# Kernel optimization log

Hardware: AMD Instinct MI355X
Metric: run time of the kernel (lower is better)

The kernel has to match this reference:

```python
import jax, jax.numpy as jnp
import numpy as np

B, T, F, H1, H2 = 16384, 10, 500, 256, 100  # batch, seq_len, noise_dim/seq_len, LSTM units, GRU units


def setup_inputs() -> dict:
    key = jax.random.key(0)
    ks = jax.random.split(key, 10)
    s = 0.02  # small init so relu activations stay bounded over time steps
    return {
        "noise": jax.random.normal(ks[0], (B, T * F), dtype=jnp.float32),
        "Wx_lstm": jax.random.normal(ks[1], (F, 4 * H1), dtype=jnp.float32) * s,
        "Wh_lstm": jax.random.normal(ks[2], (H1, 4 * H1), dtype=jnp.float32) * s,
        "b_lstm": jnp.zeros((4 * H1,), dtype=jnp.float32),
        "Wx_gru": jax.random.normal(ks[3], (H1, 3 * H2), dtype=jnp.float32) * s,
        "Wh_gru": jax.random.normal(ks[4], (H2, 3 * H2), dtype=jnp.float32) * s,
        "b_in_gru": jnp.zeros((3 * H2,), dtype=jnp.float32),
        "b_rec_gru": jnp.zeros((3 * H2,), dtype=jnp.float32),
        "Wd": jax.random.normal(ks[5], (H2, T), dtype=jnp.float32) * s,
        "bd": jnp.zeros((T,), dtype=jnp.float32),
    }


def _lstm(x, Wx, Wh, b):
    # x: [T, B, F]; Keras LSTM with activation='relu', recurrent_activation='sigmoid'
    Bn = x.shape[1]
    H = Wh.shape[0]
    def step(carry, x_t):
        h, c = carry
        z = x_t @ Wx + h @ Wh + b  # [B, 4H]
        i, f, g, o = jnp.split(z, 4, axis=-1)  # Keras gate order: i, f, c, o
        i = jax.nn.sigmoid(i)
        f = jax.nn.sigmoid(f)
        g = jax.nn.relu(g)
        o = jax.nn.sigmoid(o)
        c = f * c + i * g
        h = o * jax.nn.relu(c)
        return (h, c), h
    h0 = jnp.zeros((Bn, H), dtype=x.dtype)
    (_, _), hs = jax.lax.scan(step, (h0, h0), x)
    return hs  # [T, B, H]


def _gru(x, Wx, Wh, b_in, b_rec):
    # x: [T, B, H1]; Keras GRU (reset_after=True) with activation='relu'
    Bn = x.shape[1]
    H = Wh.shape[0]
    def step(h, x_t):
        mx = x_t @ Wx + b_in    # [B, 3H]
        mh = h @ Wh + b_rec     # [B, 3H]
        xz, xr, xh = jnp.split(mx, 3, axis=-1)  # Keras gate order: z, r, h
        hz, hr, hh = jnp.split(mh, 3, axis=-1)
        z = jax.nn.sigmoid(xz + hz)
        r = jax.nn.sigmoid(xr + hr)
        hcand = jax.nn.relu(xh + r * hh)
        h = z * h + (1.0 - z) * hcand
        return h, None
    h0 = jnp.zeros((Bn, H), dtype=x.dtype)
    h_final, _ = jax.lax.scan(step, h0, x)
    return h_final  # [B, H]


def reference(noise, Wx_lstm, Wh_lstm, b_lstm, Wx_gru, Wh_gru, b_in_gru, b_rec_gru, Wd, bd):
    Fdim = Wx_lstm.shape[0]
    Tdim = noise.shape[1] // Fdim
    x = noise.reshape(noise.shape[0], Tdim, Fdim)      # Reshape((T, F))
    x = jnp.transpose(x, (1, 0, 2))                    # [T, B, F] for scan
    hs = _lstm(x, Wx_lstm, Wh_lstm, b_lstm)            # [T, B, 256]
    h = _gru(hs, Wx_gru, Wh_gru, b_in_gru, b_rec_gru)  # [B, 100]
    return jax.nn.relu(h @ Wd + bd)                    # [B, T]
```

## Files before the change

### kernel.cpp

```cpp
#include <hip/hip_runtime.h>

#define Bsz 16384
#define TT 10
#define FF 500
#define H1c 256
#define H2c 100

typedef _Float16 half8 __attribute__((ext_vector_type(8)));
typedef float floatx4 __attribute__((ext_vector_type(4)));

__device__ __forceinline__ float sigm(float x) { return 1.0f / (1.0f + __expf(-x)); }

#define GLOAD16(g, l) __builtin_amdgcn_global_load_lds( \
    (const __attribute__((address_space(1))) void*)(g), \
    (__attribute__((address_space(3))) void*)(l), 16, 0, 0)

__global__ __launch_bounds__(256)
void conv_all(const float* __restrict__ noise, _Float16* __restrict__ xc)
{
    const int idx = blockIdx.x * 256 + threadIdx.x;
    const int rb = idx >> 6;
    const int kc = (idx & 63) << 3;
    const int b = rb / 10;
    const int t = rb - b * 10;
    const float* src = noise + (size_t)rb * FF + kc;
    half8 v;
    if (kc + 8 <= FF) {
        float4 u0 = *(const float4*)src;
        float4 u1 = *(const float4*)(src + 4);
        v[0] = (_Float16)u0.x; v[1] = (_Float16)u0.y; v[2] = (_Float16)u0.z; v[3] = (_Float16)u0.w;
        v[4] = (_Float16)u1.x; v[5] = (_Float16)u1.y; v[6] = (_Float16)u1.z; v[7] = (_Float16)u1.w;
    } else {
        #pragma unroll
        for (int j = 0; j < 8; ++j)
            v[j] = (kc + j < FF) ? (_Float16)src[j] : (_Float16)0.f;
    }
    *(half8*)(xc + ((size_t)t * Bsz + b) * 512 + kc) = v;
}

__global__ __launch_bounds__(256)
void prep_lstm_w(const float* __restrict__ Wx, const float* __restrict__ Wh,
                 _Float16* __restrict__ WT)
{
    const int idx = blockIdx.x * 256 + threadIdx.x;
    const int np = idx / 768, k = idx % 768;
    const int A2 = np >> 8, B2 = (np >> 6) & 3, g = (np >> 4) & 3, u = np & 15;
    const int U = A2 * 64 + B2 * 16 + u;
    const int col = g * 256 + U;
    float v = 0.f;
    if (k < 512) { if (k < FF) v = Wx[(size_t)k * 1024 + col]; }
    else v = Wh[(size_t)(k - 512) * 1024 + col];
    WT[idx] = (_Float16)v;
}

__global__ __launch_bounds__(256)
void prep_gru_w(const float* __restrict__ Wxg, const float* __restrict__ Whg,
                _Float16* __restrict__ WT)
{
    const int idx = blockIdx.x * 256 + threadIdx.x;
    if (idx >= 384 * 384) return;
    const int np = idx / 384, k = idx % 384;
    const int nb = np / 96, rem = np % 96;
    const int wxx = rem / 48, g = (rem % 48) / 16, u = rem & 15;
    const int U = nb * 32 + wxx * 16 + u;
    float v = 0.f;
    if (U < H2c) {
        if (k < 256) v = Wxg[(size_t)k * 300 + g * H2c + U];
        else if (k - 256 < H2c) v = Whg[(size_t)(k - 256) * 300 + g * H2c + U];
    }
    WT[idx] = (_Float16)v;
}

__device__ __forceinline__
void lstm_tile(int bid, const _Float16* __restrict__ xct, const _Float16* __restrict__ WT,
               const float* __restrict__ bias,
               const _Float16* __restrict__ h_prev, const float* __restrict__ c_prev,
               _Float16* __restrict__ h_out, float* __restrict__ c_out,
               int first, _Float16* smem)
{
    _Float16* As = smem;
    _Float16* Bs = smem + 32768;

    const int tid = threadIdx.x;
    const int lane = tid & 63;
    const int w = tid >> 6;
    const int wy = w >> 2, wx = w & 3;
    const int xcd = bid & 7;
    const int nb = xcd >> 1;
    const int row0 = (((xcd & 1) << 5) + (bid >> 3)) * 256;

    const int fr = lane & 15;
    const int l4 = lane >> 4;
    const int sr8 = lane >> 3;
    const int qsrc = (((lane & 7) ^ (sr8 & 7)) << 3);

    floatx4 acc[8][4];
    #pragma unroll
    for (int a = 0; a < 8; ++a)
        #pragma unroll
        for (int b = 0; b < 4; ++b) acc[a][b] = (floatx4){0.f, 0.f, 0.f, 0.f};

    const int nkt = first ? 8 : 12;

    #pragma unroll
    for (int q = 0; q < 4; ++q) {
        const int r = q * 64 + w * 8;
        GLOAD16(xct + (size_t)(row0 + r + sr8) * 512 + qsrc, &As[r * 64]);
        GLOAD16(WT + (size_t)(nb * 256 + r + sr8) * 768 + qsrc, &Bs[r * 64]);
    }
    __syncthreads();

    for (int T = 0; T < nkt; ++T) {
        const int pbase = (T & 1) * 16384;
        const int sbase = pbase ^ 16384;
        const int kb2 = (T + 1) * 64;
        const bool do_stage = (T + 1 < nkt);
        const bool from_x = kb2 < 512;

        #pragma unroll
        for (int q = 0; q < 4; ++q) {
            const int mh = q >> 1, nh = q & 1;
            half8 af[4][2], bf[2][2];
            #pragma unroll
            for (int j = 0; j < 4; ++j) {
                const int row = wy * 128 + (mh * 4 + j) * 16 + fr;
                #pragma unroll
                for (int ks = 0; ks < 2; ++ks) {
                    const int ch = (ks * 4 + l4) ^ (fr & 7);
                    af[j][ks] = *(const half8*)&As[pbase + row * 64 + ch * 8];
                }
            }
            #pragma unroll
            for (int jn = 0; jn < 2; ++jn) {
                const int row = wx * 64 + (nh * 2 + jn) * 16 + fr;
                #pragma unroll
                for (int ks = 0; ks < 2; ++ks) {
                    const int ch = (ks * 4 + l4) ^ (fr & 7);
                    bf[jn][ks] = *(const half8*)&Bs[pbase + row * 64 + ch * 8];
                }
            }
            if (do_stage) {
                const int r = q * 64 + w * 8;
                if (from_x)
                    GLOAD16(xct + (size_t)(row0 + r + sr8) * 512 + kb2 + qsrc, &As[sbase + r * 64]);
                else
                    GLOAD16(h_prev + (size_t)(row0 + r + sr8) * 256 + (kb2 - 512) + qsrc, &As[sbase + r * 64]);
                GLOAD16(WT + (size_t)(nb * 256 + r + sr8) * 768 + kb2 + qsrc, &Bs[sbase + r * 64]);
            }
            __builtin_amdgcn_s_setprio(1);
            #pragma unroll
            for (int ks = 0; ks < 2; ++ks)
                #pragma unroll
                for (int j = 0; j < 4; ++j)
                    #pragma unroll
                    for (int jn = 0; jn < 2; ++jn)
                        acc[mh * 4 + j][nh * 2 + jn] = __builtin_amdgcn_mfma_f32_16x16x32_f16(
                            af[j][ks], bf[jn][ks], acc[mh * 4 + j][nh * 2 + jn], 0, 0, 0);
            __builtin_amdgcn_s_setprio(0);
            __builtin_amdgcn_sched_barrier(0);
        }
        __syncthreads();
    }

    const int U = nb * 64 + wx * 16 + fr;
    const float bi = bias[0 * 256 + U];
    const float bff = bias[1 * 256 + U];
    const float bg = bias[2 * 256 + U];
    const float bo = bias[3 * 256 + U];
    const int rbase = row0 + wy * 128 + l4 * 4;
    #pragma unroll
    for (int mi = 0; mi < 8; ++mi) {
        #pragma unroll
        for (int r = 0; r < 4; ++r) {
            const int row = rbase + mi * 16 + r;
            const float cp = first ? 0.f : c_prev[(size_t)row * 256 + U];
            const float zi = acc[mi][0][r] + bi;
            const float zf = acc[mi][1][r] + bff;
            const float zg = acc[mi][2][r] + bg;
            const float zo = acc[mi][3][r] + bo;
            const float ig = sigm(zi), fg = sigm(zf), og = sigm(zo);
            const float gg = fmaxf(zg, 0.f);
            const float cv = fg * cp + ig * gg;
            const float hv = og * fmaxf(cv, 0.f);
            c_out[(size_t)row * 256 + U] = cv;
            h_out[(size_t)row * 256 + U] = (_Float16)hv;
        }
    }
}

__device__ __forceinline__
void gru_tile(int bid, int first,
              const _Float16* __restrict__ h_r, const _Float16* __restrict__ g16_r,
              const _Float16* __restrict__ WTg,
              const float* __restrict__ b_in, const float* __restrict__ b_rec,
              _Float16* __restrict__ g16_w,
              _Float16* As, _Float16* Bs)
{
    const int tid = threadIdx.x;
    const int lane = tid & 63;
    const int w = tid >> 6;
    const int wq = w >> 2;
    const int wn = w & 3;
    const int rb0 = bid * 64;
    const int fr = lane & 15;
    const int l4 = lane >> 4;
    const int sr8 = lane >> 3;
    const int qsrc = (((lane & 7) ^ sr8) << 3);

    floatx4 accA[2][6], accB[2][6];
    #pragma unroll
    for (int a = 0; a < 2; ++a)
        #pragma unroll
        for (int b = 0; b < 6; ++b) {
            accA[a][b] = (floatx4){0.f, 0.f, 0.f, 0.f};
            accB[a][b] = (floatx4){0.f, 0.f, 0.f, 0.f};
        }

    const int nkt = first ? 4 : 6;
    for (int kt = 0; kt < nkt; ++kt) {
        const int kb = kt * 64;
        {
            const int r = w * 8;
            if (kt < 4)
                GLOAD16(h_r + (size_t)(rb0 + r + sr8) * 256 + kb + qsrc, &As[r * 64]);
            else
                GLOAD16(g16_r + (size_t)(rb0 + r + sr8) * 128 + (kb - 256) + qsrc, &As[r * 64]);
        }
        #pragma unroll
        for (int q = 0; q < 6; ++q) {
            const int r = q * 64 + w * 8;
            GLOAD16(WTg + (size_t)(r + sr8) * 384 + kb + qsrc, &Bs[r * 64]);
        }
        __syncthreads();
        #pragma unroll
        for (int ks = 0; ks < 2; ++ks) {
            half8 af[2], bf[6];
            const int ch0 = (ks * 4 + l4) ^ (fr & 7);
            #pragma unroll
            for (int mf = 0; mf < 2; ++mf) {
                const int row = wq * 32 + mf * 16 + fr;
                af[mf] = *(const half8*)&As[row * 64 + ch0 * 8];
            }
            #pragma unroll
            for (int nf = 0; nf < 6; ++nf) {
                const int row = wn * 96 + nf * 16 + fr;
                bf[nf] = *(const half8*)&Bs[row * 64 + ch0 * 8];
            }
            if (kt < 4) {
                #pragma unroll
                for (int mf = 0; mf < 2; ++mf)
                    #pragma unroll
                    for (int nf = 0; nf < 6; ++nf)
                        accA[mf][nf] = __builtin_amdgcn_mfma_f32_16x16x32_f16(af[mf], bf[nf], accA[mf][nf], 0, 0, 0);
            } else {
                #pragma unroll
                for (int mf = 0; mf < 2; ++mf)
                    #pragma unroll
                    for (int nf = 0; nf < 6; ++nf)
                        accB[mf][nf] = __builtin_amdgcn_mfma_f32_16x16x32_f16(af[mf], bf[nf], accB[mf][nf], 0, 0, 0);
            }
        }
        __syncthreads();
    }

    #pragma unroll
    for (int mf = 0; mf < 2; ++mf) {
        #pragma unroll
        for (int wxx = 0; wxx < 2; ++wxx) {
            const int U = wn * 32 + wxx * 16 + fr;
            const bool uv = U < H2c;
            const float bzi = uv ? b_in[U] : 0.f;
            const float bri = uv ? b_in[H2c + U] : 0.f;
            const float bhi = uv ? b_in[2 * H2c + U] : 0.f;
            const float bzr = uv ? b_rec[U] : 0.f;
            const float brr = uv ? b_rec[H2c + U] : 0.f;
            const float bhr = uv ? b_rec[2 * H2c + U] : 0.f;
            const int nf0 = wxx * 3;
            #pragma unroll
            for (int r = 0; r < 4; ++r) {
                const int row = rb0 + wq * 32 + mf * 16 + l4 * 4 + r;
                const float gp = (!first && uv) ? (float)g16_r[(size_t)row * 128 + U] : 0.f;
                const float mxz = accA[mf][nf0 + 0][r] + bzi;
                const float mxr = accA[mf][nf0 + 1][r] + bri;
                const float mxh = accA[mf][nf0 + 2][r] + bhi;
                const float mhz = accB[mf][nf0 + 0][r] + bzr;
                const float mhr = accB[mf][nf0 + 1][r] + brr;
                const float mhh = accB[mf][nf0 + 2][r] + bhr;
                const float z = sigm(mxz + mhz);
                const float rr = sigm(mxr + mhr);
                const float hc = fmaxf(mxh + rr * mhh, 0.f);
                const float g = z * gp + (1.f - z) * hc;
                g16_w[(size_t)row * 128 + U] = uv ? (_Float16)g : (_Float16)0.f;
            }
        }
    }
}

__device__ __forceinline__
void dense_tile(int bid, const _Float16* __restrict__ hg, const float* __restrict__ Wd,
                const float* __restrict__ bd, float* __restrict__ out)
{
    const int tid = threadIdx.x;
    if (tid < 64) {
        const int row = bid * 64 + tid;
        float acc[TT];
        #pragma unroll
        for (int j = 0; j < TT; ++j) acc[j] = 0.f;
        const _Float16* gr = hg + (size_t)row * 128;
        for (int k = 0; k < H2c; ++k) {
            const float xv = (float)gr[k];
            #pragma unroll
            for (int j = 0; j < TT; ++j) acc[j] += xv * Wd[k * TT + j];
        }
        #pragma unroll
        for (int j = 0; j < TT; ++j)
            out[(size_t)row * TT + j] = fmaxf(acc[j] + bd[j], 0.f);
    }
}

__global__ __launch_bounds__(512, 2)
void step_fused(const _Float16* __restrict__ xct, const _Float16* __restrict__ WTl,
                const float* __restrict__ b_l,
                const _Float16* __restrict__ h_prev, const float* __restrict__ c_prev,
                _Float16* __restrict__ h_out, float* __restrict__ c_out,
                const _Float16* __restrict__ WTg,
                const float* __restrict__ b_in, const float* __restrict__ b_rec,
                const _Float16* __restrict__ g16_r, _Float16* __restrict__ g16_w,
                int lstm_first, int gru_on, int gru_first)
{
    extern __shared__ _Float16 smem[];
    const int bid = blockIdx.x;
    lstm_tile(bid, xct, WTl, b_l, h_prev, c_prev, h_out, c_out, lstm_first, smem);
    if (gru_on)
        gru_tile(bid, gru_first, h_prev, g16_r, WTg, b_in, b_rec, g16_w,
                 smem, smem + 32768);
}

__global__ __launch_bounds__(512, 2)
void gru_dense_tail(const _Float16* __restrict__ h_r, const _Float16* __restrict__ g16_r,
                    const _Float16* __restrict__ WTg,
                    const float* __restrict__ b_in, const float* __restrict__ b_rec,
                    _Float16* __restrict__ g16_w,
                    const float* __restrict__ Wd, const float* __restrict__ bd,
                    float* __restrict__ out)
{
    __shared__ _Float16 smem[28672];
    gru_tile(blockIdx.x, 0, h_r, g16_r, WTg, b_in, b_rec, g16_w,
             smem, smem + 4096);
    __syncthreads();
    dense_tile(blockIdx.x, g16_w, Wd, bd, out);
}

extern "C" void kernel_launch(void* const* d_in, const int* in_sizes, int n_in,
                              void* d_out, int out_size, void* d_ws, size_t ws_size,
                              hipStream_t stream)
{
    const float* noise  = (const float*)d_in[0];
    const float* Wx_l   = (const float*)d_in[1];
    const float* Wh_l   = (const float*)d_in[2];
    const float* b_l    = (const float*)d_in[3];
    const float* Wx_g   = (const float*)d_in[4];
    const float* Wh_g   = (const float*)d_in[5];
    const float* b_in   = (const float*)d_in[6];
    const float* b_rec  = (const float*)d_in[7];
    const float* Wd     = (const float*)d_in[8];
    const float* bd     = (const float*)d_in[9];
    float* outf = (float*)d_out;

    char* p = (char*)d_ws;
    auto alloc = [&](size_t bytes) {
        char* r = p;
        p += (bytes + 255) & ~(size_t)255;
        return r;
    };
    _Float16* WTl  = (_Float16*)alloc((size_t)1024 * 768 * 2);
    _Float16* WTg  = (_Float16*)alloc((size_t)384 * 384 * 2);
    _Float16* xc   = (_Float16*)alloc((size_t)Bsz * TT * 512 * 2);
    _Float16* h16A = (_Float16*)alloc((size_t)Bsz * 256 * 2);
    _Float16* h16B = (_Float16*)alloc((size_t)Bsz * 256 * 2);
    float*    cA   = (float*)alloc((size_t)Bsz * 256 * 4);
    float*    cB   = (float*)alloc((size_t)Bsz * 256 * 4);
    _Float16* g16A = (_Float16*)alloc((size_t)Bsz * 128 * 2);
    _Float16* g16B = (_Float16*)alloc((size_t)Bsz * 128 * 2);

    (void)hipFuncSetAttribute((const void*)step_fused,
                              hipFuncAttributeMaxDynamicSharedMemorySize, 131072);

    conv_all<<<Bsz * TT * 64 / 256, 256, 0, stream>>>(noise, xc);
    prep_lstm_w<<<1024 * 768 / 256, 256, 0, stream>>>(Wx_l, Wh_l, WTl);
    prep_gru_w<<<(384 * 384 + 255) / 256, 256, 0, stream>>>(Wx_g, Wh_g, WTg);

    _Float16* hb[2] = {h16A, h16B};
    float*    cb[2] = {cA, cB};
    _Float16* gh[2] = {g16A, g16B};

    for (int t = 0; t < TT; ++t) {
        const int wi = t & 1, ri = (t + 1) & 1;
        step_fused<<<256, 512, 131072, stream>>>(
            xc + (size_t)t * Bsz * 512, WTl, b_l,
            hb[ri], cb[ri], hb[wi], cb[wi],
            WTg, b_in, b_rec, gh[wi], gh[ri],
            t == 0 ? 1 : 0, t >= 1 ? 1 : 0, t == 1 ? 1 : 0);
    }
    gru_dense_tail<<<256, 512, 0, stream>>>(hb[1], gh[0], WTg, b_in, b_rec,
                                            gh[1], Wd, bd, outf);
}
```

Before: 570.1 us.

## Shrink LSTM tile to 128 rows, K=32 steps, 512 blocks at higher occupancy

The LSTM tile per block is halved from 256 to 128 rows and the K step drops from 64 to 32, with a new swizzle and smaller double-buffered LDS (56KB instead of 128KB). The grid doubles to 512 blocks and launch bounds rise to 4 waves per SIMD, aiming for more occupancy and latency hiding. The GRU tile now folds the z and r recurrent products into the input accumulators and keeps only the hh accumulator separate, which cuts registers and merges the biases. GRU work still runs on only the first 256 blocks, so load is uneven across the grid, and each tile reuses its staged data less.

Measured after the change: 573.9 us. About the same (+0.7%).

```diff
diff --git a/kernel.cpp b/kernel.cpp
--- a/kernel.cpp
+++ b/kernel.cpp
@@ -79,86 +79,73 @@
                int first, _Float16* smem)
 {
     _Float16* As = smem;
-    _Float16* Bs = smem + 32768;
+    _Float16* Bs = smem + 8192;
 
     const int tid = threadIdx.x;
     const int lane = tid & 63;
     const int w = tid >> 6;
-    const int wy = w >> 2, wx = w & 3;
+    const int wy = w >> 2;
+    const int wx = w & 3;
     const int xcd = bid & 7;
     const int nb = xcd >> 1;
-    const int row0 = (((xcd & 1) << 5) + (bid >> 3)) * 256;
+    const int row0 = (((xcd & 1) << 6) + (bid >> 3)) * 128;
 
     const int fr = lane & 15;
     const int l4 = lane >> 4;
-    const int sr8 = lane >> 3;
-    const int qsrc = (((lane & 7) ^ (sr8 & 7)) << 3);
-
-    floatx4 acc[8][4];
+    const int srow = lane >> 2;
+    const int qsrc = (((lane & 3) ^ ((lane >> 3) & 3)) << 3);
+    const int rch  = ((l4 ^ ((fr >> 1) & 3)) << 3);
+
+    floatx4 acc[4][4];
     #pragma unroll
-    for (int a = 0; a < 8; ++a)
+    for (int a = 0; a < 4; ++a)
         #pragma unroll
         for (int b = 0; b < 4; ++b) acc[a][b] = (floatx4){0.f, 0.f, 0.f, 0.f};
 
-    const int nkt = first ? 8 : 12;
-
-    #pragma unroll
-    for (int q = 0; q < 4; ++q) {
-        const int r = q * 64 + w * 8;
-        GLOAD16(xct + (size_t)(row0 + r + sr8) * 512 + qsrc, &As[r * 64]);
-        GLOAD16(WT + (size_t)(nb * 256 + r + sr8) * 768 + qsrc, &Bs[r * 64]);
-    }
+    const int nkt = first ? 16 : 24;
+
+    auto STAGE = [&](int T) {
+        const int bufA = (T & 1) * 4096;
+        const int bufB = (T & 1) * 8192;
+        const int kb = T * 32;
+        const bool fx = kb < 512;
+        {
+            const int row = w * 16 + srow;
+            if (fx)
+                GLOAD16(xct + (size_t)(row0 + row) * 512 + kb + qsrc, &As[bufA + w * 512]);
+            else
+                GLOAD16(h_prev + (size_t)(row0 + row) * 256 + (kb - 512) + qsrc, &As[bufA + w * 512]);
+        }
+        #pragma unroll
+        for (int i = 0; i < 2; ++i) {
+            const int row = i * 128 + w * 16 + srow;
+            GLOAD16(WT + (size_t)(nb * 256 + row) * 768 + kb + qsrc,
+                    &Bs[bufB + (i * 128 + w * 16) * 32]);
+        }
+    };
+
+    STAGE(0);
     __syncthreads();
 
     for (int T = 0; T < nkt; ++T) {
-        const int pbase = (T & 1) * 16384;
-        const int sbase = pbase ^ 16384;
-        const int kb2 = (T + 1) * 64;
-        const bool do_stage = (T + 1 < nkt);
-        const bool from_x = kb2 < 512;
-
-        #pragma unroll
-        for (int q = 0; q < 4; ++q) {
-            const int mh = q >> 1, nh = q & 1;
-            half8 af[4][2], bf[2][2];
-            #pragma unroll
-            for (int j = 0; j < 4; ++j) {
-                const int row = wy * 128 + (mh * 4 + j) * 16 + fr;
-                #pragma unroll
-                for (int ks = 0; ks < 2; ++ks) {
-                    const int ch = (ks * 4 + l4) ^ (fr & 7);
-                    af[j][ks] = *(const half8*)&As[pbase + row * 64 + ch * 8];
-                }
-            }
-            #pragma unroll
-            for (int jn = 0; jn < 2; ++jn) {
-                const int row = wx * 64 + (nh * 2 + jn) * 16 + fr;
-                #pragma unroll
-                for (int ks = 0; ks < 2; ++ks) {
-                    const int ch = (ks * 4 + l4) ^ (fr & 7);
-                    bf[jn][ks] = *(const half8*)&Bs[pbase + row * 64 + ch * 8];
-                }
-            }
-            if (do_stage) {
-                const int r = q * 64 + w * 8;
-                if (from_x)
-                    GLOAD16(xct + (size_t)(row0 + r + sr8) * 512 + kb2 + qsrc, &As[sbase + r * 64]);
-                else
-                    GLOAD16(h_prev + (size_t)(row0 + r + sr8) * 256 + (kb2 - 512) + qsrc, &As[sbase + r * 64]);
-                GLOAD16(WT + (size_t)(nb * 256 + r + sr8) * 768 + kb2 + qsrc, &Bs[sbase + r * 64]);
-            }
-            __builtin_amdgcn_s_setprio(1);
-            #pragma unroll
-            for (int ks = 0; ks < 2; ++ks)
-                #pragma unroll
-                for (int j = 0; j < 4; ++j)
-                    #pragma unroll
-                    for (int jn = 0; jn < 2; ++jn)
-                        acc[mh * 4 + j][nh * 2 + jn] = __builtin_amdgcn_mfma_f32_16x16x32_f16(
-                            af[j][ks], bf[jn][ks], acc[mh * 4 + j][nh * 2 + jn], 0, 0, 0);
-            __builtin_amdgcn_s_setprio(0);
-            __builtin_amdgcn_sched_barrier(0);
-        }
+        const int bA = (T & 1) * 4096;
+        const int bB = (T & 1) * 8192;
+        half8 af[4], bf[4];
+        #pragma unroll
+        for (int j = 0; j < 4; ++j)
+            af[j] = *(const half8*)&As[bA + (wy * 64 + j * 16 + fr) * 32 + rch];
+        #pragma unroll
+        for (int n = 0; n < 4; ++n)
+            bf[n] = *(const half8*)&Bs[bB + (wx * 64 + n * 16 + fr) * 32 + rch];
+        if (T + 1 < nkt) STAGE(T + 1);
+        __builtin_amdgcn_s_setprio(1);
+        #pragma unroll
+        for (int j = 0; j < 4; ++j)
+            #pragma unroll
+            for (int n = 0; n < 4; ++n)
+                acc[j][n] = __builtin_amdgcn_mfma_f32_16x16x32_f16(af[j], bf[n], acc[j][n], 0, 0, 0);
+        __builtin_amdgcn_s_setprio(0);
+        __builtin_amdgcn_sched_barrier(0);
         __syncthreads();
     }
 
@@ -167,9 +154,9 @@
     const float bff = bias[1 * 256 + U];
     const float bg = bias[2 * 256 + U];
     const float bo = bias[3 * 256 + U];
-    const int rbase = row0 + wy * 128 + l4 * 4;
+    const int rbase = row0 + wy * 64 + l4 * 4;
     #pragma unroll
-    for (int mi = 0; mi < 8; ++mi) {
+    for (int mi = 0; mi < 4; ++mi) {
         #pragma unroll
         for (int r = 0; r < 4; ++r) {
             const int row = rbase + mi * 16 + r;
@@ -207,14 +194,14 @@
     const int sr8 = lane >> 3;
     const int qsrc = (((lane & 7) ^ sr8) << 3);
 
-    floatx4 accA[2][6], accB[2][6];
+    floatx4 accA[2][6], accB[2][2];
     #pragma unroll
-    for (int a = 0; a < 2; ++a)
-        #pragma unroll
-        for (int b = 0; b < 6; ++b) {
-            accA[a][b] = (floatx4){0.f, 0.f, 0.f, 0.f};
-            accB[a][b] = (floatx4){0.f, 0.f, 0.f, 0.f};
-        }
+    for (int a = 0; a < 2; ++a) {
+        #pragma unroll
+        for (int b = 0; b < 6; ++b) accA[a][b] = (floatx4){0.f, 0.f, 0.f, 0.f};
+        accB[a][0] = (floatx4){0.f, 0.f, 0.f, 0.f};
+        accB[a][1] = (floatx4){0.f, 0.f, 0.f, 0.f};
+    }
 
     const int nkt = first ? 4 : 6;
     for (int kt = 0; kt < nkt; ++kt) {
@@ -254,10 +241,14 @@
                         accA[mf][nf] = __builtin_amdgcn_mfma_f32_16x16x32_f16(af[mf], bf[nf], accA[mf][nf], 0, 0, 0);
             } else {
                 #pragma unroll
-                for (int mf = 0; mf < 2; ++mf)
-                    #pragma unroll
-                    for (int nf = 0; nf < 6; ++nf)
-                        accB[mf][nf] = __builtin_amdgcn_mfma_f32_16x16x32_f16(af[mf], bf[nf], accB[mf][nf], 0, 0, 0);
+                for (int mf = 0; mf < 2; ++mf) {
+                    accA[mf][0] = __builtin_amdgcn_mfma_f32_16x16x32_f16(af[mf], bf[0], accA[mf][0], 0, 0, 0);
+                    accA[mf][1] = __builtin_amdgcn_mfma_f32_16x16x32_f16(af[mf], bf[1], accA[mf][1], 0, 0, 0);
+                    accB[mf][0] = __builtin_amdgcn_mfma_f32_16x16x32_f16(af[mf], bf[2], accB[mf][0], 0, 0, 0);
+                    accA[mf][3] = __builtin_amdgcn_mfma_f32_16x16x32_f16(af[mf], bf[3], accA[mf][3], 0, 0, 0);
+                    accA[mf][4] = __builtin_amdgcn_mfma_f32_16x16x32_f16(af[mf], bf[4], accA[mf][4], 0, 0, 0);
+                    accB[mf][1] = __builtin_amdgcn_mfma_f32_16x16x32_f16(af[mf], bf[5], accB[mf][1], 0, 0, 0);
+                }
             }
         }
         __syncthreads();
@@ -269,25 +260,19 @@
         for (int wxx = 0; wxx < 2; ++wxx) {
             const int U = wn * 32 + wxx * 16 + fr;
             const bool uv = U < H2c;
-            const float bzi = uv ? b_in[U] : 0.f;
-            const float bri = uv ? b_in[H2c + U] : 0.f;
+            const float bz = uv ? (b_in[U] + b_rec[U]) : 0.f;
+            const float br = uv ? (b_in[H2c + U] + b_rec[H2c + U]) : 0.f;
             const float bhi = uv ? b_in[2 * H2c + U] : 0.f;
-            const float bzr = uv ? b_rec[U] : 0.f;
-            const float brr = uv ? b_rec[H2c + U] : 0.f;
             const float bhr = uv ? b_rec[2 * H2c + U] : 0.f;
             const int nf0 = wxx * 3;
             #pragma unroll
             for (int r = 0; r < 4; ++r) {
                 const int row = rb0 + wq * 32 + mf * 16 + l4 * 4 + r;
                 const float gp = (!first && uv) ? (float)g16_r[(size_t)row * 128 + U] : 0.f;
-                const float mxz = accA[mf][nf0 + 0][r] + bzi;
-                const float mxr = accA[mf][nf0 + 1][r] + bri;
+                const float z = sigm(accA[mf][nf0 + 0][r] + bz);
+                const float rr = sigm(accA[mf][nf0 + 1][r] + br);
                 const float mxh = accA[mf][nf0 + 2][r] + bhi;
-                const float mhz = accB[mf][nf0 + 0][r] + bzr;
-                const float mhr = accB[mf][nf0 + 1][r] + brr;
-                const float mhh = accB[mf][nf0 + 2][r] + bhr;
-                const float z = sigm(mxz + mhz);
-                const float rr = sigm(mxr + mhr);
+                const float mhh = accB[mf][wxx][r] + bhr;
                 const float hc = fmaxf(mxh + rr * mhh, 0.f);
                 const float g = z * gp + (1.f - z) * hc;
                 g16_w[(size_t)row * 128 + U] = uv ? (_Float16)g : (_Float16)0.f;
@@ -318,7 +303,7 @@
     }
 }
 
-__global__ __launch_bounds__(512, 2)
+__global__ __launch_bounds__(512, 4)
 void step_fused(const _Float16* __restrict__ xct, const _Float16* __restrict__ WTl,
                 const float* __restrict__ b_l,
                 const _Float16* __restrict__ h_prev, const float* __restrict__ c_prev,
@@ -331,9 +316,9 @@
     extern __shared__ _Float16 smem[];
     const int bid = blockIdx.x;
     lstm_tile(bid, xct, WTl, b_l, h_prev, c_prev, h_out, c_out, lstm_first, smem);
-    if (gru_on)
+    if (gru_on && bid < 256)
         gru_tile(bid, gru_first, h_prev, g16_r, WTg, b_in, b_rec, g16_w,
-                 smem, smem + 32768);
+                 smem, smem + 4096);
 }
 
 __global__ __launch_bounds__(512, 2)
@@ -384,7 +369,7 @@
     _Float16* g16B = (_Float16*)alloc((size_t)Bsz * 128 * 2);
 
     (void)hipFuncSetAttribute((const void*)step_fused,
-                              hipFuncAttributeMaxDynamicSharedMemorySize, 131072);
+                              hipFuncAttributeMaxDynamicSharedMemorySize, 57344);
 
     conv_all<<<Bsz * TT * 64 / 256, 256, 0, stream>>>(noise, xc);
     prep_lstm_w<<<1024 * 768 / 256, 256, 0, stream>>>(Wx_l, Wh_l, WTl);
@@ -396,7 +381,7 @@
 
     for (int t = 0; t < TT; ++t) {
         const int wi = t & 1, ri = (t + 1) & 1;
-        step_fused<<<256, 512, 131072, stream>>>(
+        step_fused<<<512, 512, 57344, stream>>>(
             xc + (size_t)t * Bsz * 512, WTl, b_l,
             hb[ri], cb[ri], hb[wi], cb[wi],
             WTg, b_in, b_rec, gh[wi], gh[ri],
```

## Fuse noise fp32-to-fp16 conversion into LSTM tile loads, drop conv_all pass

Applied to the files above, without the earlier changes.

Removes the separate conversion kernel and the fp16 staging buffer. Each LSTM step now reads fp32 noise directly into registers, converts it to fp16 and writes it into swizzled shared memory. The next tile's loads are issued before the MFMA loop and stored to LDS after it. This avoids a full extra write and read of the converted input in global memory, at the cost of more fp32 traffic, extra register pressure and synchronous LDS stores instead of async global-to-LDS loads.

After: 989.5 us. 73.6% more time.

```diff
diff --git a/kernel.cpp b/kernel.cpp
--- a/kernel.cpp
+++ b/kernel.cpp
@@ -14,29 +14,6 @@
 #define GLOAD16(g, l) __builtin_amdgcn_global_load_lds( \
     (const __attribute__((address_space(1))) void*)(g), \
     (__attribute__((address_space(3))) void*)(l), 16, 0, 0)
-
-__global__ __launch_bounds__(256)
-void conv_all(const float* __restrict__ noise, _Float16* __restrict__ xc)
-{
-    const int idx = blockIdx.x * 256 + threadIdx.x;
-    const int rb = idx >> 6;
-    const int kc = (idx & 63) << 3;
-    const int b = rb / 10;
-    const int t = rb - b * 10;
-    const float* src = noise + (size_t)rb * FF + kc;
-    half8 v;
-    if (kc + 8 <= FF) {
-        float4 u0 = *(const float4*)src;
-        float4 u1 = *(const float4*)(src + 4);
-        v[0] = (_Float16)u0.x; v[1] = (_Float16)u0.y; v[2] = (_Float16)u0.z; v[3] = (_Float16)u0.w;
-        v[4] = (_Float16)u1.x; v[5] = (_Float16)u1.y; v[6] = (_Float16)u1.z; v[7] = (_Float16)u1.w;
-    } else {
-        #pragma unroll
-        for (int j = 0; j < 8; ++j)
-            v[j] = (kc + j < FF) ? (_Float16)src[j] : (_Float16)0.f;
-    }
-    *(half8*)(xc + ((size_t)t * Bsz + b) * 512 + kc) = v;
-}
 
 __global__ __launch_bounds__(256)
 void prep_lstm_w(const float* __restrict__ Wx, const float* __restrict__ Wh,
@@ -72,7 +49,8 @@
 }
 
 __device__ __forceinline__
-void lstm_tile(int bid, const _Float16* __restrict__ xct, const _Float16* __restrict__ WT,
+void lstm_tile(int bid, const float* __restrict__ noise, int t,
+               const _Float16* __restrict__ WT,
                const float* __restrict__ bias,
                const _Float16* __restrict__ h_prev, const float* __restrict__ c_prev,
                _Float16* __restrict__ h_out, float* __restrict__ c_out,
@@ -94,6 +72,9 @@
     const int sr8 = lane >> 3;
     const int qsrc = (((lane & 7) ^ (sr8 & 7)) << 3);
 
+    const int arow = tid >> 1;
+    const int kh = (tid & 1) * 32;
+
     floatx4 acc[8][4];
     #pragma unroll
     for (int a = 0; a < 8; ++a)
@@ -102,11 +83,26 @@
 
     const int nkt = first ? 8 : 12;
 
-    #pragma unroll
-    for (int q = 0; q < 4; ++q) {
-        const int r = q * 64 + w * 8;
-        GLOAD16(xct + (size_t)(row0 + r + sr8) * 512 + qsrc, &As[r * 64]);
-        GLOAD16(WT + (size_t)(nb * 256 + r + sr8) * 768 + qsrc, &Bs[r * 64]);
+    {
+        #pragma unroll
+        for (int q = 0; q < 4; ++q) {
+            const int r = q * 64 + w * 8;
+            GLOAD16(WT + (size_t)(nb * 256 + r + sr8) * 768 + qsrc, &Bs[r * 64]);
+        }
+        const float* srow = noise + (size_t)(row0 + arow) * (TT * FF) + t * FF + kh;
+        float4 xv[8];
+        #pragma unroll
+        for (int j = 0; j < 8; ++j) xv[j] = *(const float4*)(srow + j * 4);
+        #pragma unroll
+        for (int cj = 0; cj < 4; ++cj) {
+            half8 hv;
+            hv[0] = (_Float16)xv[2 * cj].x;     hv[1] = (_Float16)xv[2 * cj].y;
+            hv[2] = (_Float16)xv[2 * cj].z;     hv[3] = (_Float16)xv[2 * cj].w;
+            hv[4] = (_Float16)xv[2 * cj + 1].x; hv[5] = (_Float16)xv[2 * cj + 1].y;
+            hv[6] = (_Float16)xv[2 * cj + 1].z; hv[7] = (_Float16)xv[2 * cj + 1].w;
+            const int c = (tid & 1) * 4 + cj;
+            *(half8*)&As[(size_t)arow * 64 + (c ^ (arow & 7)) * 8] = hv;
+        }
     }
     __syncthreads();
 
@@ -115,7 +111,17 @@
         const int sbase = pbase ^ 16384;
         const int kb2 = (T + 1) * 64;
         const bool do_stage = (T + 1 < nkt);
-        const bool from_x = kb2 < 512;
+        const bool nx_x = kb2 < 512;
+
+        float4 xv[8];
+        if (do_stage && nx_x) {
+            const float* srow = noise + (size_t)(row0 + arow) * (TT * FF) + t * FF + kb2 + kh;
+            #pragma unroll
+            for (int j = 0; j < 8; ++j) {
+                if (kb2 + kh + j * 4 + 3 < FF) xv[j] = *(const float4*)(srow + j * 4);
+                else xv[j] = make_float4(0.f, 0.f, 0.f, 0.f);
+            }
+        }
 
         #pragma unroll
         for (int q = 0; q < 4; ++q) {
@@ -141,9 +147,7 @@
             }
             if (do_stage) {
                 const int r = q * 64 + w * 8;
-                if (from_x)
-                    GLOAD16(xct + (size_t)(row0 + r + sr8) * 512 + kb2 + qsrc, &As[sbase + r * 64]);
-                else
+                if (!nx_x)
                     GLOAD16(h_prev + (size_t)(row0 + r + sr8) * 256 + (kb2 - 512) + qsrc, &As[sbase + r * 64]);
                 GLOAD16(WT + (size_t)(nb * 256 + r + sr8) * 768 + kb2 + qsrc, &Bs[sbase + r * 64]);
             }
@@ -158,6 +162,19 @@
                             af[j][ks], bf[jn][ks], acc[mh * 4 + j][nh * 2 + jn], 0, 0, 0);
             __builtin_amdgcn_s_setprio(0);
             __builtin_amdgcn_sched_barrier(0);
+        }
+
+        if (do_stage && nx_x) {
+            #pragma unroll
+            for (int cj = 0; cj < 4; ++cj) {
+                half8 hv;
+                hv[0] = (_Float16)xv[2 * cj].x;     hv[1] = (_Float16)xv[2 * cj].y;
+                hv[2] = (_Float16)xv[2 * cj].z;     hv[3] = (_Float16)xv[2 * cj].w;
+                hv[4] = (_Float16)xv[2 * cj + 1].x; hv[5] = (_Float16)xv[2 * cj + 1].y;
+                hv[6] = (_Float16)xv[2 * cj + 1].z; hv[7] = (_Float16)xv[2 * cj + 1].w;
+                const int c = (tid & 1) * 4 + cj;
+                *(half8*)&As[sbase + (size_t)arow * 64 + (c ^ (arow & 7)) * 8] = hv;
+            }
         }
         __syncthreads();
     }
@@ -319,7 +336,8 @@
 }
 
 __global__ __launch_bounds__(512, 2)
-void step_fused(const _Float16* __restrict__ xct, const _Float16* __restrict__ WTl,
+void step_fused(const float* __restrict__ noise, int t,
+                const _Float16* __restrict__ WTl,
                 const float* __restrict__ b_l,
                 const _Float16* __restrict__ h_prev, const float* __restrict__ c_prev,
                 _Float16* __restrict__ h_out, float* __restrict__ c_out,
@@ -330,7 +348,7 @@
 {
     extern __shared__ _Float16 smem[];
     const int bid = blockIdx.x;
-    lstm_tile(bid, xct, WTl, b_l, h_prev, c_prev, h_out, c_out, lstm_first, smem);
+    lstm_tile(bid, noise, t, WTl, b_l, h_prev, c_prev, h_out, c_out, lstm_first, smem);
     if (gru_on)
         gru_tile(bid, gru_first, h_prev, g16_r, WTg, b_in, b_rec, g16_w,
                  smem, smem + 32768);
@@ -375,7 +393,6 @@
     };
     _Float16* WTl  = (_Float16*)alloc((size_t)1024 * 768 * 2);
     _Float16* WTg  = (_Float16*)alloc((size_t)384 * 384 * 2);
-    _Float16* xc   = (_Float16*)alloc((size_t)Bsz * TT * 512 * 2);
     _Float16* h16A = (_Float16*)alloc((size_t)Bsz * 256 * 2);
     _Float16* h16B = (_Float16*)alloc((size_t)Bsz * 256 * 2);
     float*    cA   = (float*)alloc((size_t)Bsz * 256 * 4);
@@ -386,7 +403,6 @@
     (void)hipFuncSetAttribute((const void*)step_fused,
                               hipFuncAttributeMaxDynamicSharedMemorySize, 131072);
 
-    conv_all<<<Bsz * TT * 64 / 256, 256, 0, stream>>>(noise, xc);
     prep_lstm_w<<<1024 * 768 / 256, 256, 0, stream>>>(Wx_l, Wh_l, WTl);
     prep_gru_w<<<(384 * 384 + 255) / 256, 256, 0, stream>>>(Wx_g, Wh_g, WTg);
 
@@ -397,7 +413,7 @@
     for (int t = 0; t < TT; ++t) {
         const int wi = t & 1, ri = (t + 1) & 1;
         step_fused<<<256, 512, 131072, stream>>>(
-            xc + (size_t)t * Bsz * 512, WTl, b_l,
+            noise, t, WTl, b_l,
             hb[ri], cb[ri], hb[wi], cb[wi],
             WTg, b_in, b_rec, gh[wi], gh[ri],
             t == 0 ? 1 : 0, t >= 1 ? 1 : 0, t == 1 ? 1 : 0);
```

## Fuse all LSTM/GRU timesteps into one persistent kernel with LDS-resident state

Applied to the files above, without the earlier changes.

Replaces the per-timestep launches (ten step kernels plus a GRU/dense tail) with a single kernel. Each block owns 64 batch rows and runs all timesteps of the LSTM, the GRU and the final dense layer. The LSTM c state stays in registers and the h and GRU states stay in LDS, which removes the global round trips and launch overheads between steps. The cost is that every block re-streams the full LSTM and GRU weight matrices from global or L2 memory at every step, with smaller M tiles (64 rows) and more barriers. Only 256 blocks run, so occupancy and MFMA efficiency per block may drop.

Measured after the change: 906.0 us. 58.9% more time.

```diff
diff --git a/kernel.cpp b/kernel.cpp
--- a/kernel.cpp
+++ b/kernel.cpp
@@ -71,284 +71,247 @@
     WT[idx] = (_Float16)v;
 }
 
-__device__ __forceinline__
-void lstm_tile(int bid, const _Float16* __restrict__ xct, const _Float16* __restrict__ WT,
-               const float* __restrict__ bias,
-               const _Float16* __restrict__ h_prev, const float* __restrict__ c_prev,
-               _Float16* __restrict__ h_out, float* __restrict__ c_out,
-               int first, _Float16* smem)
-{
-    _Float16* As = smem;
-    _Float16* Bs = smem + 32768;
+__global__ __launch_bounds__(512, 2)
+void rnn_all(const _Float16* __restrict__ xc, const _Float16* __restrict__ WTl,
+             const float* __restrict__ b_l, const _Float16* __restrict__ WTg,
+             const float* __restrict__ b_in, const float* __restrict__ b_rec,
+             const float* __restrict__ Wd, const float* __restrict__ bd,
+             float* __restrict__ out)
+{
+    extern __shared__ _Float16 smem[];
+    _Float16* hL  = smem;
+    _Float16* gL  = smem + 16384;
+    _Float16* AsX = smem + 24576;
+    _Float16* Bst = smem + 32768;
 
     const int tid = threadIdx.x;
     const int lane = tid & 63;
     const int w = tid >> 6;
     const int wy = w >> 2, wx = w & 3;
-    const int xcd = bid & 7;
-    const int nb = xcd >> 1;
-    const int row0 = (((xcd & 1) << 5) + (bid >> 3)) * 256;
-
-    const int fr = lane & 15;
-    const int l4 = lane >> 4;
-    const int sr8 = lane >> 3;
-    const int qsrc = (((lane & 7) ^ (sr8 & 7)) << 3);
-
-    floatx4 acc[8][4];
-    #pragma unroll
-    for (int a = 0; a < 8; ++a)
-        #pragma unroll
-        for (int b = 0; b < 4; ++b) acc[a][b] = (floatx4){0.f, 0.f, 0.f, 0.f};
-
-    const int nkt = first ? 8 : 12;
-
-    #pragma unroll
-    for (int q = 0; q < 4; ++q) {
-        const int r = q * 64 + w * 8;
-        GLOAD16(xct + (size_t)(row0 + r + sr8) * 512 + qsrc, &As[r * 64]);
-        GLOAD16(WT + (size_t)(nb * 256 + r + sr8) * 768 + qsrc, &Bs[r * 64]);
-    }
-    __syncthreads();
-
-    for (int T = 0; T < nkt; ++T) {
-        const int pbase = (T & 1) * 16384;
-        const int sbase = pbase ^ 16384;
-        const int kb2 = (T + 1) * 64;
-        const bool do_stage = (T + 1 < nkt);
-        const bool from_x = kb2 < 512;
-
-        #pragma unroll
-        for (int q = 0; q < 4; ++q) {
-            const int mh = q >> 1, nh = q & 1;
-            half8 af[4][2], bf[2][2];
-            #pragma unroll
-            for (int j = 0; j < 4; ++j) {
-                const int row = wy * 128 + (mh * 4 + j) * 16 + fr;
-                #pragma unroll
-                for (int ks = 0; ks < 2; ++ks) {
-                    const int ch = (ks * 4 + l4) ^ (fr & 7);
-                    af[j][ks] = *(const half8*)&As[pbase + row * 64 + ch * 8];
-                }
-            }
-            #pragma unroll
-            for (int jn = 0; jn < 2; ++jn) {
-                const int row = wx * 64 + (nh * 2 + jn) * 16 + fr;
-                #pragma unroll
-                for (int ks = 0; ks < 2; ++ks) {
-                    const int ch = (ks * 4 + l4) ^ (fr & 7);
-                    bf[jn][ks] = *(const half8*)&Bs[pbase + row * 64 + ch * 8];
-                }
-            }
-            if (do_stage) {
-                const int r = q * 64 + w * 8;
-                if (from_x)
-                    GLOAD16(xct + (size_t)(row0 + r + sr8) * 512 + kb2 + qsrc, &As[sbase + r * 64]);
-                else
-                    GLOAD16(h_prev + (size_t)(row0 + r + sr8) * 256 + (kb2 - 512) + qsrc, &As[sbase + r * 64]);
-                GLOAD16(WT + (size_t)(nb * 256 + r + sr8) * 768 + kb2 + qsrc, &Bs[sbase + r * 64]);
-            }
-            __builtin_amdgcn_s_setprio(1);
-            #pragma unroll
-            for (int ks = 0; ks < 2; ++ks)
-                #pragma unroll
-                for (int j = 0; j < 4; ++j)
-                    #pragma unroll
-                    for (int jn = 0; jn < 2; ++jn)
-                        acc[mh * 4 + j][nh * 2 + jn] = __builtin_amdgcn_mfma_f32_16x16x32_f16(
-                            af[j][ks], bf[jn][ks], acc[mh * 4 + j][nh * 2 + jn], 0, 0, 0);
-            __builtin_amdgcn_s_setprio(0);
-            __builtin_amdgcn_sched_barrier(0);
-        }
-        __syncthreads();
-    }
-
-    const int U = nb * 64 + wx * 16 + fr;
-    const float bi = bias[0 * 256 + U];
-    const float bff = bias[1 * 256 + U];
-    const float bg = bias[2 * 256 + U];
-    const float bo = bias[3 * 256 + U];
-    const int rbase = row0 + wy * 128 + l4 * 4;
-    #pragma unroll
-    for (int mi = 0; mi < 8; ++mi) {
-        #pragma unroll
-        for (int r = 0; r < 4; ++r) {
-            const int row = rbase + mi * 16 + r;
-            const float cp = first ? 0.f : c_prev[(size_t)row * 256 + U];
-            const float zi = acc[mi][0][r] + bi;
-            const float zf = acc[mi][1][r] + bff;
-            const float zg = acc[mi][2][r] + bg;
-            const float zo = acc[mi][3][r] + bo;
-            const float ig = sigm(zi), fg = sigm(zf), og = sigm(zo);
-            const float gg = fmaxf(zg, 0.f);
-            const float cv = fg * cp + ig * gg;
-            const float hv = og * fmaxf(cv, 0.f);
-            c_out[(size_t)row * 256 + U] = cv;
-            h_out[(size_t)row * 256 + U] = (_Float16)hv;
-        }
-    }
-}
-
-__device__ __forceinline__
-void gru_tile(int bid, int first,
-              const _Float16* __restrict__ h_r, const _Float16* __restrict__ g16_r,
-              const _Float16* __restrict__ WTg,
-              const float* __restrict__ b_in, const float* __restrict__ b_rec,
-              _Float16* __restrict__ g16_w,
-              _Float16* As, _Float16* Bs)
-{
-    const int tid = threadIdx.x;
-    const int lane = tid & 63;
-    const int w = tid >> 6;
-    const int wq = w >> 2;
-    const int wn = w & 3;
-    const int rb0 = bid * 64;
+    const int rb0 = blockIdx.x * 64;
+
     const int fr = lane & 15;
     const int l4 = lane >> 4;
     const int sr8 = lane >> 3;
     const int qsrc = (((lane & 7) ^ sr8) << 3);
 
-    floatx4 accA[2][6], accB[2][6];
+    floatx4 c_state[4][2];
     #pragma unroll
-    for (int a = 0; a < 2; ++a)
-        #pragma unroll
-        for (int b = 0; b < 6; ++b) {
-            accA[a][b] = (floatx4){0.f, 0.f, 0.f, 0.f};
-            accB[a][b] = (floatx4){0.f, 0.f, 0.f, 0.f};
-        }
-
-    const int nkt = first ? 4 : 6;
-    for (int kt = 0; kt < nkt; ++kt) {
-        const int kb = kt * 64;
-        {
-            const int r = w * 8;
-            if (kt < 4)
-                GLOAD16(h_r + (size_t)(rb0 + r + sr8) * 256 + kb + qsrc, &As[r * 64]);
-            else
-                GLOAD16(g16_r + (size_t)(rb0 + r + sr8) * 128 + (kb - 256) + qsrc, &As[r * 64]);
-        }
-        #pragma unroll
-        for (int q = 0; q < 6; ++q) {
-            const int r = q * 64 + w * 8;
-            GLOAD16(WTg + (size_t)(r + sr8) * 384 + kb + qsrc, &Bs[r * 64]);
+    for (int nc = 0; nc < 4; ++nc) {
+        c_state[nc][0] = (floatx4){0.f, 0.f, 0.f, 0.f};
+        c_state[nc][1] = (floatx4){0.f, 0.f, 0.f, 0.f};
+    }
+
+    for (int s = 0; s < TT; ++s) {
+        const int nktL = (s == 0) ? 8 : 12;
+        floatx4 accL[4][2][4];
+        #pragma unroll
+        for (int nc = 0; nc < 4; ++nc)
+            #pragma unroll
+            for (int j = 0; j < 2; ++j)
+                #pragma unroll
+                for (int g = 0; g < 4; ++g)
+                    accL[nc][j][g] = (floatx4){0.f, 0.f, 0.f, 0.f};
+
+        #pragma unroll
+        for (int nc = 0; nc < 4; ++nc) {
+            #pragma unroll
+            for (int q = 0; q < 4; ++q) {
+                const int r = q * 64 + w * 8;
+                GLOAD16(WTl + (size_t)(nc * 256 + r + sr8) * 768 + qsrc, &Bst[r * 64]);
+            }
+            {
+                const int r = w * 8;
+                GLOAD16(xc + ((size_t)s * Bsz + rb0 + r + sr8) * 512 + qsrc, &AsX[r * 64]);
+            }
+            __syncthreads();
+
+            for (int T = 0; T < nktL; ++T) {
+                const int pb = T & 1;
+                const int sb = pb ^ 1;
+                const int kb2 = (T + 1) * 64;
+                const bool stB = (T + 1 < nktL);
+                const bool stX = stB && (kb2 < 512);
+
+                half8 af[2][2], bf[4][2];
+                #pragma unroll
+                for (int j = 0; j < 2; ++j) {
+                    const int row = wy * 32 + j * 16 + fr;
+                    #pragma unroll
+                    for (int ks = 0; ks < 2; ++ks) {
+                        const int ch = (ks * 4 + l4) ^ (fr & 7);
+                        af[j][ks] = (T < 8)
+                            ? *(const half8*)&AsX[pb * 4096 + row * 64 + ch * 8]
+                            : *(const half8*)&hL[(T - 8) * 4096 + row * 64 + ch * 8];
+                    }
+                }
+                #pragma unroll
+                for (int g = 0; g < 4; ++g) {
+                    const int row = wx * 64 + g * 16 + fr;
+                    #pragma unroll
+                    for (int ks = 0; ks < 2; ++ks) {
+                        const int ch = (ks * 4 + l4) ^ (fr & 7);
+                        bf[g][ks] = *(const half8*)&Bst[pb * 16384 + row * 64 + ch * 8];
+                    }
+                }
+                if (stB) {
+                    #pragma unroll
+                    for (int q = 0; q < 4; ++q) {
+                        const int r = q * 64 + w * 8;
+                        GLOAD16(WTl + (size_t)(nc * 256 + r + sr8) * 768 + kb2 + qsrc,
+                                &Bst[sb * 16384 + r * 64]);
+                    }
+                }
+                if (stX) {
+                    const int r = w * 8;
+                    GLOAD16(xc + ((size_t)s * Bsz + rb0 + r + sr8) * 512 + kb2 + qsrc,
+                            &AsX[sb * 4096 + r * 64]);
+                }
+                __builtin_amdgcn_s_setprio(1);
+                #pragma unroll
+                for (int ks = 0; ks < 2; ++ks)
+                    #pragma unroll
+                    for (int j = 0; j < 2; ++j)
+                        #pragma unroll
+                        for (int g = 0; g < 4; ++g)
+                            accL[nc][j][g] = __builtin_amdgcn_mfma_f32_16x16x32_f16(
+                                af[j][ks], bf[g][ks], accL[nc][j][g], 0, 0, 0);
+                __builtin_amdgcn_s_setprio(0);
+                __syncthreads();
+            }
+        }
+
+        #pragma unroll
+        for (int nc = 0; nc < 4; ++nc) {
+            const int U = nc * 64 + wx * 16 + fr;
+            const float bi  = b_l[U];
+            const float bff = b_l[256 + U];
+            const float bg  = b_l[512 + U];
+            const float bo  = b_l[768 + U];
+            #pragma unroll
+            for (int j = 0; j < 2; ++j) {
+                #pragma unroll
+                for (int rr = 0; rr < 4; ++rr) {
+                    const int row = wy * 32 + j * 16 + l4 * 4 + rr;
+                    const float cp = c_state[nc][j][rr];
+                    const float zi = accL[nc][j][0][rr] + bi;
+                    const float zf = accL[nc][j][1][rr] + bff;
+                    const float zg = accL[nc][j][2][rr] + bg;
+                    const float zo = accL[nc][j][3][rr] + bo;
+                    const float ig = sigm(zi), fg = sigm(zf), og = sigm(zo);
+                    const float gg = fmaxf(zg, 0.f);
+                    const float cv = fg * cp + ig * gg;
+                    const float hv = og * fmaxf(cv, 0.f);
+                    c_state[nc][j][rr] = cv;
+                    hL[nc * 4096 + row * 64 + ((((U >> 3) & 7) ^ (row & 7)) << 3) + (U & 7)]
+                        = (_Float16)hv;
+                }
+            }
         }
         __syncthreads();
-        #pragma unroll
-        for (int ks = 0; ks < 2; ++ks) {
-            half8 af[2], bf[6];
-            const int ch0 = (ks * 4 + l4) ^ (fr & 7);
-            #pragma unroll
-            for (int mf = 0; mf < 2; ++mf) {
-                const int row = wq * 32 + mf * 16 + fr;
-                af[mf] = *(const half8*)&As[row * 64 + ch0 * 8];
-            }
-            #pragma unroll
-            for (int nf = 0; nf < 6; ++nf) {
-                const int row = wn * 96 + nf * 16 + fr;
-                bf[nf] = *(const half8*)&Bs[row * 64 + ch0 * 8];
-            }
-            if (kt < 4) {
-                #pragma unroll
-                for (int mf = 0; mf < 2; ++mf)
-                    #pragma unroll
-                    for (int nf = 0; nf < 6; ++nf)
-                        accA[mf][nf] = __builtin_amdgcn_mfma_f32_16x16x32_f16(af[mf], bf[nf], accA[mf][nf], 0, 0, 0);
-            } else {
-                #pragma unroll
-                for (int mf = 0; mf < 2; ++mf)
-                    #pragma unroll
-                    for (int nf = 0; nf < 6; ++nf)
-                        accB[mf][nf] = __builtin_amdgcn_mfma_f32_16x16x32_f16(af[mf], bf[nf], accB[mf][nf], 0, 0, 0);
+
+        const int nktG = (s == 0) ? 4 : 6;
+        floatx4 gAc[2][6], gBc[2][6];
+        #pragma unroll
+        for (int a = 0; a < 2; ++a)
+            #pragma unroll
+            for (int b = 0; b < 6; ++b) {
+                gAc[a][b] = (floatx4){0.f, 0.f, 0.f, 0.f};
+                gBc[a][b] = (floatx4){0.f, 0.f, 0.f, 0.f};
+            }
+
+        for (int kt = 0; kt < nktG; ++kt) {
+            #pragma unroll
+            for (int q = 0; q < 6; ++q) {
+                const int r = q * 64 + w * 8;
+                GLOAD16(WTg + (size_t)(r + sr8) * 384 + kt * 64 + qsrc, &Bst[r * 64]);
+            }
+            __syncthreads();
+            const _Float16* Asrc = (kt < 4) ? &hL[kt * 4096] : &gL[(kt - 4) * 4096];
+            #pragma unroll
+            for (int ks = 0; ks < 2; ++ks) {
+                half8 af2[2], bf2[6];
+                const int ch = (ks * 4 + l4) ^ (fr & 7);
+                #pragma unroll
+                for (int mf = 0; mf < 2; ++mf) {
+                    const int row = wy * 32 + mf * 16 + fr;
+                    af2[mf] = *(const half8*)&Asrc[row * 64 + ch * 8];
+                }
+                #pragma unroll
+                for (int nf = 0; nf < 6; ++nf) {
+                    const int row = wx * 96 + nf * 16 + fr;
+                    bf2[nf] = *(const half8*)&Bst[row * 64 + ch * 8];
+                }
+                if (kt < 4) {
+                    #pragma unroll
+                    for (int mf = 0; mf < 2; ++mf)
+                        #pragma unroll
+                        for (int nf = 0; nf < 6; ++nf)
+                            gAc[mf][nf] = __builtin_amdgcn_mfma_f32_16x16x32_f16(
+                                af2[mf], bf2[nf], gAc[mf][nf], 0, 0, 0);
+                } else {
+                    #pragma unroll
+                    for (int mf = 0; mf < 2; ++mf)
+                        #pragma unroll
+                        for (int nf = 0; nf < 6; ++nf)
+                            gBc[mf][nf] = __builtin_amdgcn_mfma_f32_16x16x32_f16(
+                                af2[mf], bf2[nf], gBc[mf][nf], 0, 0, 0);
+                }
+            }
+            __syncthreads();
+        }
+
+        #pragma unroll
+        for (int mf = 0; mf < 2; ++mf) {
+            #pragma unroll
+            for (int wxx = 0; wxx < 2; ++wxx) {
+                const int U = wx * 32 + wxx * 16 + fr;
+                const bool uv = U < H2c;
+                const float bzi = uv ? b_in[U] : 0.f;
+                const float bri = uv ? b_in[H2c + U] : 0.f;
+                const float bhi = uv ? b_in[2 * H2c + U] : 0.f;
+                const float bzr = uv ? b_rec[U] : 0.f;
+                const float brr = uv ? b_rec[H2c + U] : 0.f;
+                const float bhr = uv ? b_rec[2 * H2c + U] : 0.f;
+                const int nf0 = wxx * 3;
+                #pragma unroll
+                for (int rr = 0; rr < 4; ++rr) {
+                    const int row = wy * 32 + mf * 16 + l4 * 4 + rr;
+                    const size_t gaddr = (U >> 6) * 4096 + row * 64 +
+                        ((((U >> 3) & 7) ^ (row & 7)) << 3) + (U & 7);
+                    const float gp = (s == 0) ? 0.f : (uv ? (float)gL[gaddr] : 0.f);
+                    const float mxz = gAc[mf][nf0 + 0][rr] + bzi;
+                    const float mxr = gAc[mf][nf0 + 1][rr] + bri;
+                    const float mxh = gAc[mf][nf0 + 2][rr] + bhi;
+                    const float mhz = gBc[mf][nf0 + 0][rr] + bzr;
+                    const float mhr = gBc[mf][nf0 + 1][rr] + brr;
+                    const float mhh = gBc[mf][nf0 + 2][rr] + bhr;
+                    const float z = sigm(mxz + mhz);
+                    const float r2 = sigm(mxr + mhr);
+                    const float hc = fmaxf(mxh + r2 * mhh, 0.f);
+                    const float g = z * gp + (1.f - z) * hc;
+                    gL[gaddr] = uv ? (_Float16)g : (_Float16)0.f;
+                }
             }
         }
         __syncthreads();
     }
 
-    #pragma unroll
-    for (int mf = 0; mf < 2; ++mf) {
-        #pragma unroll
-        for (int wxx = 0; wxx < 2; ++wxx) {
-            const int U = wn * 32 + wxx * 16 + fr;
-            const bool uv = U < H2c;
-            const float bzi = uv ? b_in[U] : 0.f;
-            const float bri = uv ? b_in[H2c + U] : 0.f;
-            const float bhi = uv ? b_in[2 * H2c + U] : 0.f;
-            const float bzr = uv ? b_rec[U] : 0.f;
-            const float brr = uv ? b_rec[H2c + U] : 0.f;
-            const float bhr = uv ? b_rec[2 * H2c + U] : 0.f;
-            const int nf0 = wxx * 3;
-            #pragma unroll
-            for (int r = 0; r < 4; ++r) {
-                const int row = rb0 + wq * 32 + mf * 16 + l4 * 4 + r;
-                const float gp = (!first && uv) ? (float)g16_r[(size_t)row * 128 + U] : 0.f;
-                const float mxz = accA[mf][nf0 + 0][r] + bzi;
-                const float mxr = accA[mf][nf0 + 1][r] + bri;
-                const float mxh = accA[mf][nf0 + 2][r] + bhi;
-                const float mhz = accB[mf][nf0 + 0][r] + bzr;
-                const float mhr = accB[mf][nf0 + 1][r] + brr;
-                const float mhh = accB[mf][nf0 + 2][r] + bhr;
-                const float z = sigm(mxz + mhz);
-                const float rr = sigm(mxr + mhr);
-                const float hc = fmaxf(mxh + rr * mhh, 0.f);
-                const float g = z * gp + (1.f - z) * hc;
-                g16_w[(size_t)row * 128 + U] = uv ? (_Float16)g : (_Float16)0.f;
-            }
-        }
-    }
-}
-
-__device__ __forceinline__
-void dense_tile(int bid, const _Float16* __restrict__ hg, const float* __restrict__ Wd,
-                const float* __restrict__ bd, float* __restrict__ out)
-{
-    const int tid = threadIdx.x;
     if (tid < 64) {
-        const int row = bid * 64 + tid;
+        const int row = tid;
         float acc[TT];
         #pragma unroll
         for (int j = 0; j < TT; ++j) acc[j] = 0.f;
-        const _Float16* gr = hg + (size_t)row * 128;
         for (int k = 0; k < H2c; ++k) {
-            const float xv = (float)gr[k];
+            const float xv = (float)gL[(k >> 6) * 4096 + row * 64 +
+                ((((k >> 3) & 7) ^ (row & 7)) << 3) + (k & 7)];
             #pragma unroll
             for (int j = 0; j < TT; ++j) acc[j] += xv * Wd[k * TT + j];
         }
         #pragma unroll
         for (int j = 0; j < TT; ++j)
-            out[(size_t)row * TT + j] = fmaxf(acc[j] + bd[j], 0.f);
-    }
-}
-
-__global__ __launch_bounds__(512, 2)
-void step_fused(const _Float16* __restrict__ xct, const _Float16* __restrict__ WTl,
-                const float* __restrict__ b_l,
-                const _Float16* __restrict__ h_prev, const float* __restrict__ c_prev,
-                _Float16* __restrict__ h_out, float* __restrict__ c_out,
-                const _Float16* __restrict__ WTg,
-                const float* __restrict__ b_in, const float* __restrict__ b_rec,
-                const _Float16* __restrict__ g16_r, _Float16* __restrict__ g16_w,
-                int lstm_first, int gru_on, int gru_first)
-{
-    extern __shared__ _Float16 smem[];
-    const int bid = blockIdx.x;
-    lstm_tile(bid, xct, WTl, b_l, h_prev, c_prev, h_out, c_out, lstm_first, smem);
-    if (gru_on)
-        gru_tile(bid, gru_first, h_prev, g16_r, WTg, b_in, b_rec, g16_w,
-                 smem, smem + 32768);
-}
-
-__global__ __launch_bounds__(512, 2)
-void gru_dense_tail(const _Float16* __restrict__ h_r, const _Float16* __restrict__ g16_r,
-                    const _Float16* __restrict__ WTg,
-                    const float* __restrict__ b_in, const float* __restrict__ b_rec,
-                    _Float16* __restrict__ g16_w,
-                    const float* __restrict__ Wd, const float* __restrict__ bd,
-                    float* __restrict__ out)
-{
-    __shared__ _Float16 smem[28672];
-    gru_tile(blockIdx.x, 0, h_r, g16_r, WTg, b_in, b_rec, g16_w,
-             smem, smem + 4096);
-    __syncthreads();
-    dense_tile(blockIdx.x, g16_w, Wd, bd, out);
+            out[(size_t)(rb0 + row) * TT + j] = fmaxf(acc[j] + bd[j], 0.f);
+    }
 }
 
 extern "C" void kernel_launch(void* const* d_in, const int* in_sizes, int n_in,
@@ -373,35 +336,16 @@
         p += (bytes + 255) & ~(size_t)255;
         return r;
     };
-    _Float16* WTl  = (_Float16*)alloc((size_t)1024 * 768 * 2);
-    _Float16* WTg  = (_Float16*)alloc((size_t)384 * 384 * 2);
-    _Float16* xc   = (_Float16*)alloc((size_t)Bsz * TT * 512 * 2);
-    _Float16* h16A = (_Float16*)alloc((size_t)Bsz * 256 * 2);
-    _Float16* h16B = (_Float16*)alloc((size_t)Bsz * 256 * 2);
-    float*    cA   = (float*)alloc((size_t)Bsz * 256 * 4);
-    float*    cB   = (float*)alloc((size_t)Bsz * 256 * 4);
-    _Float16* g16A = (_Float16*)alloc((size_t)Bsz * 128 * 2);
-    _Float16* g16B = (_Float16*)alloc((size_t)Bsz * 128 * 2);
-
-    (void)hipFuncSetAttribute((const void*)step_fused,
+    _Float16* WTl = (_Float16*)alloc((size_t)1024 * 768 * 2);
+    _Float16* WTg = (_Float16*)alloc((size_t)384 * 384 * 2);
+    _Float16* xc  = (_Float16*)alloc((size_t)Bsz * TT * 512 * 2);
+
+    (void)hipFuncSetAttribute((const void*)rnn_all,
                               hipFuncAttributeMaxDynamicSharedMemorySize, 131072);
 
     conv_all<<<Bsz * TT * 64 / 256, 256, 0, stream>>>(noise, xc);
     prep_lstm_w<<<1024 * 768 / 256, 256, 0, stream>>>(Wx_l, Wh_l, WTl);
     prep_gru_w<<<(384 * 384 + 255) / 256, 256, 0, stream>>>(Wx_g, Wh_g, WTg);
 
-    _Float16* hb[2] = {h16A, h16B};
-    float*    cb[2] = {cA, cB};
-    _Float16* gh[2] = {g16A, g16B};
-
-    for (int t = 0; t < TT; ++t) {
-        const int wi = t & 1, ri = (t + 1) & 1;
-        step_fused<<<256, 512, 131072, stream>>>(
-            xc + (size_t)t * Bsz * 512, WTl, b_l,
-            hb[ri], cb[ri], hb[wi], cb[wi],
-            WTg, b_in, b_rec, gh[wi], gh[ri],
-            t == 0 ? 1 : 0, t >= 1 ? 1 : 0, t == 1 ? 1 : 0);
-    }
-    gru_dense_tail<<<256, 512, 0, stream>>>(hb[1], gh[0], WTg, b_in, b_rec,
-                                            gh[1], Wd, bd, outf);
-}
+    rnn_all<<<256, 512, 131072, stream>>>(xc, WTl, b_l, WTg, b_in, b_rec, Wd, bd, outf);
+}
```
